# Performance work log

Measured on AMD Instinct MI355X. Metric: run time of the kernel, lower is better.

The kernel has to match this reference:

```python
import jax, jax.numpy as jnp
import numpy as np

BLOCK = 32
LAYER_MAX = 6.0
E2M1_BOUNDS = jnp.array([0.25, 0.75, 1.25, 1.75, 2.5, 3.5, 5.0], dtype=jnp.float32)
E2M1_VALUES = jnp.array([0.0, 0.5, 1.0, 1.5, 2.0, 3.0, 4.0, 6.0], dtype=jnp.float32)


def setup_inputs() -> dict:
    key = jax.random.key(0)
    k1, k2 = jax.random.split(key)
    out_f, in_f = 8192, 8192
    num_blocks = out_f * (in_f // BLOCK)
    weight_fp = jax.random.normal(k1, (out_f, in_f), dtype=jnp.float32) * 0.05
    # eps_param is the learned pre-tanh block offset (one scalar per block)
    eps_param = jax.random.normal(k2, (num_blocks,), dtype=jnp.float32) * 0.2
    return {"weight_fp": weight_fp, "eps_param": eps_param}


def reference(weight_fp, eps_param):
    out_f, in_f = weight_fp.shape
    nb = in_f // BLOCK
    # [out_f, nb, BLOCK]
    w_blocks = weight_fp.reshape(out_f, nb, BLOCK)
    amax = jnp.max(jnp.abs(w_blocks), axis=-1, keepdims=True)
    descale = amax / LAYER_MAX
    # e8m0 scale: exp2(ceil(max(log2(descale), -127)))
    e8m0_scale = jnp.ceil(jnp.maximum(jnp.log2(descale), -127.0))
    scale = jnp.exp2(e8m0_scale)  # [out_f, nb, 1]
    w_norm = w_blocks / scale
    # block epsilon offset: eps = 0.5 * tanh(p) in (-0.5, 0.5)
    eps_base = 0.5 * jnp.tanh(eps_param)  # [out_f*nb]
    eps_blocks = eps_base.reshape(out_f, nb, 1)
    abs_shifted = jnp.maximum(jnp.abs(w_norm) + eps_blocks, 0.0)
    sign = jnp.sign(w_norm)
    # matches torch (2 - sign) // 2 : 0 for positive, 1 for negative/zero
    sign_bit = jnp.floor((2.0 - sign) / 2.0)
    # threshold-count encode against E2M1 bounds -> ord in [0, 7]
    ord_ = jnp.sum(abs_shifted[..., None] > E2M1_BOUNDS, axis=-1)  # int32 [out_f, nb, BLOCK]
    encoded = (sign_bit.astype(jnp.int32) * 8 + ord_).astype(jnp.uint8)
    # dequantize via values-table gather
    mantissa = E2M1_VALUES[ord_]
    signed_mantissa = mantissa * (1.0 - 2.0 * sign_bit)
    deq_weight = (signed_mantissa * scale).reshape(out_f, in_f)
    e8m0_scale_uint8 = (e8m0_scale + 127.0).astype(jnp.uint8)  # [out_f, nb, 1]
    return (deq_weight, encoded.reshape(out_f, in_f), e8m0_scale_uint8, eps_base)
```

## Files before the change

### kernel.cpp

```cpp
#include <hip/hip_runtime.h>
#include <math.h>


typedef float f32x4 __attribute__((ext_vector_type(4)));

constexpr unsigned long long NELEM = 8192ull * 8192ull;
constexpr unsigned           NBLK  = (unsigned)(NELEM / 32);

__global__ __launch_bounds__(256) void e2m1_quant_kernel(
    const float* __restrict__ w,
    const float* __restrict__ eps_p,
    float* __restrict__ out)
{
    const unsigned tid  = blockIdx.x * 256u + threadIdx.x;
    const unsigned b    = tid >> 2;
    const unsigned sub  = tid & 3u;
    const unsigned base = b * 32u + sub * 4u;

    const f32x4* wp = reinterpret_cast<const f32x4*>(w + base);
    const f32x4 w0 = __builtin_nontemporal_load(wp);
    const f32x4 w1 = __builtin_nontemporal_load(wp + 4);
    const float p  = eps_p[b];

    float a = fmaxf(fmaxf(fmaxf(fabsf(w0[0]), fabsf(w0[1])),
                          fmaxf(fabsf(w0[2]), fabsf(w0[3]))),
                    fmaxf(fmaxf(fabsf(w1[0]), fabsf(w1[1])),
                          fmaxf(fabsf(w1[2]), fabsf(w1[3]))));
    a = fmaxf(a, __shfl_xor(a, 1));
    a = fmaxf(a, __shfl_xor(a, 2));

    const float descale = a / 6.0f;
    const unsigned du = __float_as_uint(descale);
    const int ex = (int)(du >> 23);
    int e = ex - 127 + ((du & 0x7fffffu) ? 1 : 0);
    e = (ex == 0) ? -127 : e;
    e = (e < -127) ? -127 : e;
    const float rscale = ldexpf(1.0f, -e);

    const float t  = fabsf(p);
    const float em = __expf(-2.0f * t);
    const float th = (1.0f - em) * __builtin_amdgcn_rcpf(1.0f + em);
    const float ep = 0.5f * copysignf(th, p);

    const float vals[8] = {w0[0], w0[1], w0[2], w0[3],
                           w1[0], w1[1], w1[2], w1[3]};
    float dq[8], ec[8];

#pragma unroll
    for (int i = 0; i < 8; ++i) {
        const float wn = vals[i] * rscale;
        const float as = fmaxf(fabsf(wn) + ep, 0.0f);
        const int o = (as > 0.25f) + (as > 0.75f) + (as > 1.25f) + (as > 1.75f)
                    + (as > 2.5f)  + (as > 3.5f)  + (as > 5.0f);
        const bool neg = (wn <= 0.0f);
        const int nib = (int)((0xC8643210u >> (o * 4)) & 0xFu);
        dq[i] = ldexpf((float)(neg ? -nib : nib), e - 1);
        ec[i] = (float)(o | (neg ? 8 : 0));
    }

    f32x4* dptr = reinterpret_cast<f32x4*>(out + base);
    __builtin_nontemporal_store((f32x4){dq[0], dq[1], dq[2], dq[3]}, dptr);
    __builtin_nontemporal_store((f32x4){dq[4], dq[5], dq[6], dq[7]}, dptr + 4);
    f32x4* eptr = reinterpret_cast<f32x4*>(out + NELEM + base);
    __builtin_nontemporal_store((f32x4){ec[0], ec[1], ec[2], ec[3]}, eptr);
    __builtin_nontemporal_store((f32x4){ec[4], ec[5], ec[6], ec[7]}, eptr + 4);

    if (sub == 0) {
        out[2 * NELEM + b]        = (float)(e + 127);
        out[2 * NELEM + NBLK + b] = ep;
    }
}

extern "C" void kernel_launch(void* const* d_in, const int* in_sizes, int n_in,
                              void* d_out, int out_size, void* d_ws, size_t ws_size,
                              hipStream_t stream) {
    const float* w     = (const float*)d_in[0];
    const float* eps_p = (const float*)d_in[1];
    float* out = (float*)d_out;

    const unsigned n_threads = NBLK * 4u;
    const int block = 256;
    const int grid  = (int)(n_threads / (unsigned)block);
    e2m1_quant_kernel<<<grid, block, 0, stream>>>(w, eps_p, out);
}
```

Baseline: 706.4 us.

## Remap threads to contiguous float4 per lane with two half-array blocks

Each thread now loads one float4 from each half of the weight array, so consecutive lanes read consecutive 16-byte chunks and a wave's accesses are fully contiguous. The old layout gave each lane two float4s strided by 16 bytes. The block max reduction now spans 8 lanes via an extra shuffle. Nontemporal loads and stores are replaced with ordinary ones, which changes cache behaviour for this streaming kernel.

Result: no change. 707.3 us (+0.1%).

```diff
diff --git a/kernel.cpp b/kernel.cpp
--- a/kernel.cpp
+++ b/kernel.cpp
@@ -6,28 +6,17 @@
 
 constexpr unsigned long long NELEM = 8192ull * 8192ull;
 constexpr unsigned           NBLK  = (unsigned)(NELEM / 32);
+constexpr unsigned           NTHREADS = (unsigned)(NELEM / 8);
 
-__global__ __launch_bounds__(256) void e2m1_quant_kernel(
-    const float* __restrict__ w,
-    const float* __restrict__ eps_p,
-    float* __restrict__ out)
+__device__ __forceinline__ void process4(
+    const f32x4 wv, const float p,
+    float& e_f, float& ep, f32x4& dq, f32x4& ec)
 {
-    const unsigned tid  = blockIdx.x * 256u + threadIdx.x;
-    const unsigned b    = tid >> 2;
-    const unsigned sub  = tid & 3u;
-    const unsigned base = b * 32u + sub * 4u;
-
-    const f32x4* wp = reinterpret_cast<const f32x4*>(w + base);
-    const f32x4 w0 = __builtin_nontemporal_load(wp);
-    const f32x4 w1 = __builtin_nontemporal_load(wp + 4);
-    const float p  = eps_p[b];
-
-    float a = fmaxf(fmaxf(fmaxf(fabsf(w0[0]), fabsf(w0[1])),
-                          fmaxf(fabsf(w0[2]), fabsf(w0[3]))),
-                    fmaxf(fmaxf(fabsf(w1[0]), fabsf(w1[1])),
-                          fmaxf(fabsf(w1[2]), fabsf(w1[3]))));
+    float a = fmaxf(fmaxf(fabsf(wv[0]), fabsf(wv[1])),
+                    fmaxf(fabsf(wv[2]), fabsf(wv[3])));
     a = fmaxf(a, __shfl_xor(a, 1));
     a = fmaxf(a, __shfl_xor(a, 2));
+    a = fmaxf(a, __shfl_xor(a, 4));
 
     const float descale = a / 6.0f;
     const unsigned du = __float_as_uint(descale);
@@ -35,20 +24,17 @@
     int e = ex - 127 + ((du & 0x7fffffu) ? 1 : 0);
     e = (ex == 0) ? -127 : e;
     e = (e < -127) ? -127 : e;
+    e_f = (float)(e + 127);
     const float rscale = ldexpf(1.0f, -e);
 
     const float t  = fabsf(p);
     const float em = __expf(-2.0f * t);
     const float th = (1.0f - em) * __builtin_amdgcn_rcpf(1.0f + em);
-    const float ep = 0.5f * copysignf(th, p);
-
-    const float vals[8] = {w0[0], w0[1], w0[2], w0[3],
-                           w1[0], w1[1], w1[2], w1[3]};
-    float dq[8], ec[8];
+    ep = 0.5f * copysignf(th, p);
 
 #pragma unroll
-    for (int i = 0; i < 8; ++i) {
-        const float wn = vals[i] * rscale;
+    for (int i = 0; i < 4; ++i) {
+        const float wn = wv[i] * rscale;
         const float as = fmaxf(fabsf(wn) + ep, 0.0f);
         const int o = (as > 0.25f) + (as > 0.75f) + (as > 1.25f) + (as > 1.75f)
                     + (as > 2.5f)  + (as > 3.5f)  + (as > 5.0f);
@@ -57,17 +43,39 @@
         dq[i] = ldexpf((float)(neg ? -nib : nib), e - 1);
         ec[i] = (float)(o | (neg ? 8 : 0));
     }
+}
 
-    f32x4* dptr = reinterpret_cast<f32x4*>(out + base);
-    __builtin_nontemporal_store((f32x4){dq[0], dq[1], dq[2], dq[3]}, dptr);
-    __builtin_nontemporal_store((f32x4){dq[4], dq[5], dq[6], dq[7]}, dptr + 4);
-    f32x4* eptr = reinterpret_cast<f32x4*>(out + NELEM + base);
-    __builtin_nontemporal_store((f32x4){ec[0], ec[1], ec[2], ec[3]}, eptr);
-    __builtin_nontemporal_store((f32x4){ec[4], ec[5], ec[6], ec[7]}, eptr + 4);
+__global__ __launch_bounds__(256) void e2m1_quant_kernel(
+    const float* __restrict__ w,
+    const float* __restrict__ eps_p,
+    float* __restrict__ out)
+{
+    const unsigned tid = blockIdx.x * 256u + threadIdx.x;
+    const unsigned b0  = tid >> 3;
+    const unsigned b1  = b0 + NBLK / 2;
+    const unsigned long long off0 = 4ull * tid;
+    const unsigned long long off1 = off0 + NELEM / 2;
 
-    if (sub == 0) {
-        out[2 * NELEM + b]        = (float)(e + 127);
-        out[2 * NELEM + NBLK + b] = ep;
+    const f32x4 v0 = *reinterpret_cast<const f32x4*>(w + off0);
+    const f32x4 v1 = *reinterpret_cast<const f32x4*>(w + off1);
+    const float p0 = eps_p[b0];
+    const float p1 = eps_p[b1];
+
+    float e0f, e1f, ep0, ep1;
+    f32x4 dq0, dq1, ec0, ec1;
+    process4(v0, p0, e0f, ep0, dq0, ec0);
+    process4(v1, p1, e1f, ep1, dq1, ec1);
+
+    *reinterpret_cast<f32x4*>(out + off0) = dq0;
+    *reinterpret_cast<f32x4*>(out + off1) = dq1;
+    *reinterpret_cast<f32x4*>(out + NELEM + off0) = ec0;
+    *reinterpret_cast<f32x4*>(out + NELEM + off1) = ec1;
+
+    if ((tid & 7u) == 0) {
+        out[2 * NELEM + b0]        = e0f;
+        out[2 * NELEM + b1]        = e1f;
+        out[2 * NELEM + NBLK + b0] = ep0;
+        out[2 * NELEM + NBLK + b1] = ep1;
     }
 }
 
@@ -78,8 +86,7 @@
     const float* eps_p = (const float*)d_in[1];
     float* out = (float*)d_out;
 
-    const unsigned n_threads = NBLK * 4u;
     const int block = 256;
-    const int grid  = (int)(n_threads / (unsigned)block);
+    const int grid  = (int)(NTHREADS / (unsigned)block);
     e2m1_quant_kernel<<<grid, block, 0, stream>>>(w, eps_p, out);
 }
```
